# Performance work log

Measured on AMD Instinct MI355X. Metric: run time of the kernel, lower is better.

## Reference

```python
import jax, jax.numpy as jnp
import numpy as np

N_EXPERTS = 16
NUM_SHARDS = 1
CAPACITY_FACTOR = 1.25
EPS = 0.01


def setup_inputs() -> dict:
    key = jax.random.key(0)
    k1, k2, k3 = jax.random.split(key, 3)
    C, T, D = 4, 4096, 1024
    E = N_EXPERTS * NUM_SHARDS
    inputs = jax.random.normal(k1, (C, T, D), dtype=jnp.float32)
    # trunc-normal router weight, std = (initializer_factor / ((D + E)/2))**0.5
    std = (1.0 / ((D + E) / 2.0)) ** 0.5
    router_weight = jax.random.truncated_normal(k2, -2.0, 2.0, (E, D), dtype=jnp.float32) * std
    # multiplicative jitter in [1-eps, 1+eps)
    noise = (1.0 - EPS) + 2.0 * EPS * jax.random.uniform(k3, (C, T, D), dtype=jnp.float32)
    return {"inputs": inputs, "router_weight": router_weight, "noise": noise}


def reference(inputs, router_weight, noise):
    C, T, D = inputs.shape
    E = N_EXPERTS * NUM_SHARDS
    expert_capacity = max(int(CAPACITY_FACTOR * T // N_EXPERTS), 1)

    x = inputs.astype(jnp.float32) * noise                      # gate inputs with jitter
    router_logits = jnp.einsum('ctd,ed->cte', x, router_weight)  # [C,T,E]
    router_probs = jax.nn.softmax(router_logits, axis=-1)
    expert_gate = jnp.max(router_probs, axis=-1)                 # [C,T]
    expert_index = jnp.argmax(router_probs, axis=-1)             # [C,T] int

    expert_mask = jax.nn.one_hot(expert_index, E, dtype=jnp.float32)  # [C,T,E]

    # load-balancing aux loss (before capacity truncation)
    density1 = expert_mask.mean(axis=1)          # [C,E]
    density1_proxy = router_probs.mean(axis=1)   # [C,E]
    aux_loss = (density1 * density1_proxy).sum() * E

    # capacity-limited position tracking
    position_in_expert = jnp.cumsum(expert_mask, axis=1) * expert_mask            # [C,T,E]
    expert_mask = expert_mask * (position_in_expert.astype(jnp.int32) < expert_capacity)
    expert_mask_flat = expert_mask.sum(axis=-1)                                    # [C,T]
    position_in_expert = (jnp.cumsum(expert_mask, axis=1) * expert_mask).astype(jnp.int32)
    expert_gate = expert_gate * expert_mask_flat

    # Faithful replication of torch scatter_(dim=1) on a [C,T,E,1] tensor with
    # index shape [C,T,1,1]: only the (e=0, cap=0) slice is written, at token
    # position == expert_index[c,t].
    c_idx = jnp.arange(C)[:, None]
    expert_index_inf = jnp.zeros((C, T, E, 1), jnp.float32).at[c_idx, expert_index, 0, 0].set(1.0)

    # one-hot over capacity slot (scatter along dim 3)
    position_inf = jax.nn.one_hot(position_in_expert, expert_capacity, dtype=jnp.float32)  # [C,T,E,cap]

    combine_tensor = (expert_gate[:, :, None, None]
                      * expert_mask_flat[:, :, None, None]
                      * expert_index_inf
                      * position_inf)
    dispatch_tensor = combine_tensor.astype(bool)
    return dispatch_tensor, combine_tensor, aux_loss
```

## Files before the change

### kernel.cpp

```cpp
#include <hip/hip_runtime.h>
#include <math.h>

#define C_DIM 4
#define T_DIM 4096
#define D_DIM 1024
#define E_DIM 16
#define CAP   320
#define CT    (C_DIM * T_DIM)
#define OUT_ONE ((size_t)CT * E_DIM * CAP)

#define NBLOCKS 1024
#define N4      ((2 * OUT_ONE) / 4)
#define F4_PER_BLOCK (N4 / NBLOCKS)


__global__ __launch_bounds__(256) void fused_router_fill_kernel(
    const float* __restrict__ in, const float* __restrict__ w,
    const float* __restrict__ noise, float* __restrict__ gate,
    int* __restrict__ index, float* __restrict__ auxpart,
    int* __restrict__ counts, float4* __restrict__ out4)
{
    __shared__ float psum[E_DIM];
    __shared__ int   hcnt[E_DIM];
    const int tid  = threadIdx.x;
    if (tid < E_DIM) { psum[tid] = 0.0f; hcnt[tid] = 0; }
    __syncthreads();

    const int wave = tid >> 6;
    const int lane = tid & 63;
    const int g0   = blockIdx.x * 16 + wave * 4;

    float acc[4][16];
    #pragma unroll
    for (int tk = 0; tk < 4; ++tk)
        #pragma unroll
        for (int e = 0; e < 16; ++e)
            acc[tk][e] = 0.0f;

    #pragma unroll
    for (int r = 0; r < 4; ++r) {
        const int d0 = r * 256 + lane * 4;
        float4 x[4];
        #pragma unroll
        for (int tk = 0; tk < 4; ++tk) {
            const float4 a = *(const float4*)(in    + (size_t)(g0 + tk) * D_DIM + d0);
            const float4 n = *(const float4*)(noise + (size_t)(g0 + tk) * D_DIM + d0);
            x[tk] = make_float4(a.x * n.x, a.y * n.y, a.z * n.z, a.w * n.w);
        }
        #pragma unroll
        for (int e = 0; e < 16; ++e) {
            const float4 wv = *(const float4*)(w + e * D_DIM + d0);
            #pragma unroll
            for (int tk = 0; tk < 4; ++tk) {
                acc[tk][e] += x[tk].x * wv.x + x[tk].y * wv.y
                            + x[tk].z * wv.z + x[tk].w * wv.w;
            }
        }
    }

    #pragma unroll
    for (int tk = 0; tk < 4; ++tk)
        #pragma unroll
        for (int e = 0; e < 16; ++e)
            #pragma unroll
            for (int off = 32; off; off >>= 1)
                acc[tk][e] += __shfl_down(acc[tk][e], off, 64);

    if (lane == 0) {
        #pragma unroll
        for (int tk = 0; tk < 4; ++tk) {
            const int g = g0 + tk;
            float m = -1e30f; int am = 0;
            #pragma unroll
            for (int e = 0; e < 16; ++e)
                if (acc[tk][e] > m) { m = acc[tk][e]; am = e; }
            float p[16]; float s = 0.0f;
            #pragma unroll
            for (int e = 0; e < 16; ++e) { p[e] = __expf(acc[tk][e] - m); s += p[e]; }
            const float inv = 1.0f / s;
            gate[g]  = inv;
            index[g] = am;
            atomicAdd(&hcnt[am], 1);
            #pragma unroll
            for (int e = 0; e < 16; ++e)
                atomicAdd(&psum[e], p[e] * inv);
        }
    }
    __syncthreads();
    if (tid < 16) {
        const int c = blockIdx.x >> 8;
        atomicAdd(&auxpart[c * 16 + tid], psum[tid]);
        atomicAdd(&counts [c * 16 + tid], hcnt[tid]);
    }

    const float4 z = make_float4(0.f, 0.f, 0.f, 0.f);
    float4* dst = out4 + (size_t)blockIdx.x * F4_PER_BLOCK;
    #pragma unroll 4
    for (int i = tid; i < F4_PER_BLOCK; i += 256)
        dst[i] = z;
}

__global__ __launch_bounds__(64) void finalize_kernel(
    const float* __restrict__ gate, const int* __restrict__ index,
    const int* __restrict__ counts, const float* __restrict__ auxpart,
    float* __restrict__ out)
{
    const int id = threadIdx.x;
    const int c  = id >> 4;
    const int tp = id & 15;
    const int cnt = counts[id];

    float term = ((float)cnt * (1.0f / T_DIM)) * (auxpart[id] * (1.0f / T_DIM));

    if (cnt > 0) {
        const int g    = c * T_DIM + tp;
        const int myidx = index[g];
        int s = 0;
        if (myidx == 0) {
            int r = 0;
            for (int t = 0; t <= tp; ++t)
                r += (index[c * T_DIM + t] == 0);
            s = r;
        }
        const size_t off = ((size_t)g * E_DIM + 0) * CAP + (size_t)s;
        out[off]            = 1.0f;
        out[OUT_ONE + off]  = gate[g];
    }

    #pragma unroll
    for (int off = 32; off; off >>= 1)
        term += __shfl_down(term, off, 64);
    if (id == 0)
        out[2 * OUT_ONE] = 16.0f * term;
}

extern "C" void kernel_launch(void* const* d_in, const int* in_sizes, int n_in,
                              void* d_out, int out_size, void* d_ws, size_t ws_size,
                              hipStream_t stream) {
    const float* in    = (const float*)d_in[0];
    const float* w     = (const float*)d_in[1];
    const float* noise = (const float*)d_in[2];
    float* out = (float*)d_out;

    char* ws = (char*)d_ws;
    float* auxpart = (float*)(ws);
    int*   counts  = (int*)(ws + 256);
    float* gate    = (float*)(ws + 512);
    int*   index   = (int*)(ws + 512 + 65536);

    (void)hipMemsetAsync(ws, 0, 512, stream);

    fused_router_fill_kernel<<<dim3(NBLOCKS), dim3(256), 0, stream>>>(
        in, w, noise, gate, index, auxpart, counts, (float4*)out);
    finalize_kernel<<<dim3(1), dim3(64), 0, stream>>>(gate, index, counts, auxpart, out);
}
```

Measured before the change: 186.3 us.

## Split zero-fill into separate grid-stride kernel and use butterfly transpose-reduce for logits

The router GEMV and the large zero-fill of the dispatch/combine outputs become separate kernels. The fill now runs as its own grid-stride kernel with 4096 blocks. The 64-way shuffle-down reduction of each of the 64 accumulators is replaced by a bit-reversed butterfly reduce-scatter, which leaves one logit per lane. Softmax, argmax and the aux partial sums are then computed in parallel across lanes rather than by lane 0 alone. This cuts shuffle count and serial work, but the fill no longer overlaps with router compute inside one kernel and adds a launch.

```diff
diff --git a/kernel.cpp b/kernel.cpp
--- a/kernel.cpp
+++ b/kernel.cpp
@@ -8,21 +8,26 @@
 #define CAP   320
 #define CT    (C_DIM * T_DIM)
 #define OUT_ONE ((size_t)CT * E_DIM * CAP)
+#define N4      ((2 * OUT_ONE) / 4)
 
-#define NBLOCKS 1024
-#define N4      ((2 * OUT_ONE) / 4)
-#define F4_PER_BLOCK (N4 / NBLOCKS)
+#define ROUTER_BLOCKS 1024
+#define FILL_BLOCKS   4096
+
+__host__ __device__ constexpr int bitrev6(int i) {
+    return ((i & 1) << 5) | ((i & 2) << 3) | ((i & 4) << 1)
+         | ((i & 8) >> 1) | ((i & 16) >> 3) | ((i & 32) >> 5);
+}
 
 
-__global__ __launch_bounds__(256) void fused_router_fill_kernel(
+__global__ __launch_bounds__(256) void router_kernel(
     const float* __restrict__ in, const float* __restrict__ w,
     const float* __restrict__ noise, float* __restrict__ gate,
     int* __restrict__ index, float* __restrict__ auxpart,
-    int* __restrict__ counts, float4* __restrict__ out4)
+    int* __restrict__ counts)
 {
     __shared__ float psum[E_DIM];
     __shared__ int   hcnt[E_DIM];
-    const int tid  = threadIdx.x;
+    const int tid = threadIdx.x;
     if (tid < E_DIM) { psum[tid] = 0.0f; hcnt[tid] = 0; }
     __syncthreads();
 
@@ -30,12 +35,9 @@
     const int lane = tid & 63;
     const int g0   = blockIdx.x * 16 + wave * 4;
 
-    float acc[4][16];
+    float val[64];
     #pragma unroll
-    for (int tk = 0; tk < 4; ++tk)
-        #pragma unroll
-        for (int e = 0; e < 16; ++e)
-            acc[tk][e] = 0.0f;
+    for (int i = 0; i < 64; ++i) val[i] = 0.0f;
 
     #pragma unroll
     for (int r = 0; r < 4; ++r) {
@@ -52,52 +54,71 @@
             const float4 wv = *(const float4*)(w + e * D_DIM + d0);
             #pragma unroll
             for (int tk = 0; tk < 4; ++tk) {
-                acc[tk][e] += x[tk].x * wv.x + x[tk].y * wv.y
-                            + x[tk].z * wv.z + x[tk].w * wv.w;
+                val[bitrev6(tk * 16 + e)] += x[tk].x * wv.x + x[tk].y * wv.y
+                                           + x[tk].z * wv.z + x[tk].w * wv.w;
             }
         }
     }
 
     #pragma unroll
-    for (int tk = 0; tk < 4; ++tk)
+    for (int m = 0; m < 6; ++m) {
+        const int half = 32 >> m;
+        const int bit  = (lane >> m) & 1;
         #pragma unroll
-        for (int e = 0; e < 16; ++e)
-            #pragma unroll
-            for (int off = 32; off; off >>= 1)
-                acc[tk][e] += __shfl_down(acc[tk][e], off, 64);
-
-    if (lane == 0) {
-        #pragma unroll
-        for (int tk = 0; tk < 4; ++tk) {
-            const int g = g0 + tk;
-            float m = -1e30f; int am = 0;
-            #pragma unroll
-            for (int e = 0; e < 16; ++e)
-                if (acc[tk][e] > m) { m = acc[tk][e]; am = e; }
-            float p[16]; float s = 0.0f;
-            #pragma unroll
-            for (int e = 0; e < 16; ++e) { p[e] = __expf(acc[tk][e] - m); s += p[e]; }
-            const float inv = 1.0f / s;
-            gate[g]  = inv;
-            index[g] = am;
-            atomicAdd(&hcnt[am], 1);
-            #pragma unroll
-            for (int e = 0; e < 16; ++e)
-                atomicAdd(&psum[e], p[e] * inv);
+        for (int j = 0; j < half; ++j) {
+            const float send = bit ? val[j] : val[j + half];
+            const float recv = __shfl_xor(send, 1 << m, 64);
+            val[j] = (bit ? val[j + half] : val[j]) + recv;
         }
     }
+
+    const int tk = lane >> 4;
+    const int e  = lane & 15;
+    const float logit = val[0];
+    const int g = g0 + tk;
+
+    float mv = logit; int am = e;
+    #pragma unroll
+    for (int msk = 1; msk <= 8; msk <<= 1) {
+        const float ov = __shfl_xor(mv, msk, 64);
+        const int   oe = __shfl_xor(am, msk, 64);
+        if (ov > mv || (ov == mv && oe < am)) { mv = ov; am = oe; }
+    }
+
+    const float p = __expf(logit - mv);
+    float s = p;
+    #pragma unroll
+    for (int msk = 1; msk <= 8; msk <<= 1)
+        s += __shfl_xor(s, msk, 64);
+
+    const float inv = 1.0f / s;
+    if (e == am) {
+        gate[g]  = inv;
+        index[g] = am;
+        atomicAdd(&hcnt[am], 1);
+    }
+
+    float pn = p * inv;
+    pn += __shfl_xor(pn, 16, 64);
+    pn += __shfl_xor(pn, 32, 64);
+    if (lane < 16)
+        atomicAdd(&psum[e], pn * 0.25f * 4.0f);
+
     __syncthreads();
     if (tid < 16) {
         const int c = blockIdx.x >> 8;
         atomicAdd(&auxpart[c * 16 + tid], psum[tid]);
         atomicAdd(&counts [c * 16 + tid], hcnt[tid]);
     }
+}
 
+__global__ __launch_bounds__(256) void fill_kernel(float4* __restrict__ out4)
+{
+    const size_t stride = (size_t)FILL_BLOCKS * 256;
     const float4 z = make_float4(0.f, 0.f, 0.f, 0.f);
-    float4* dst = out4 + (size_t)blockIdx.x * F4_PER_BLOCK;
     #pragma unroll 4
-    for (int i = tid; i < F4_PER_BLOCK; i += 256)
-        dst[i] = z;
+    for (size_t i = (size_t)blockIdx.x * 256 + threadIdx.x; i < N4; i += stride)
+        out4[i] = z;
 }
 
 __global__ __launch_bounds__(64) void finalize_kernel(
@@ -113,7 +134,7 @@
     float term = ((float)cnt * (1.0f / T_DIM)) * (auxpart[id] * (1.0f / T_DIM));
 
     if (cnt > 0) {
-        const int g    = c * T_DIM + tp;
+        const int g     = c * T_DIM + tp;
         const int myidx = index[g];
         int s = 0;
         if (myidx == 0) {
@@ -150,7 +171,8 @@
 
     (void)hipMemsetAsync(ws, 0, 512, stream);
 
-    fused_router_fill_kernel<<<dim3(NBLOCKS), dim3(256), 0, stream>>>(
-        in, w, noise, gate, index, auxpart, counts, (float4*)out);
+    router_kernel<<<dim3(ROUTER_BLOCKS), dim3(256), 0, stream>>>(
+        in, w, noise, gate, index, auxpart, counts);
+    fill_kernel<<<dim3(FILL_BLOCKS), dim3(256), 0, stream>>>((float4*)out);
     finalize_kernel<<<dim3(1), dim3(64), 0, stream>>>(gate, index, counts, auxpart, out);
 }
```

Measured after the change: 215.4 us. 1.16x slower.
